# Kernel optimization log

Hardware: AMD Instinct MI355X
Metric: run time of the kernel (lower is better)

## Reference

```python
import jax, jax.numpy as jnp
import numpy as np

N, H, W = 4096, 96, 96
C0 = 0.28209479177387814
C1 = 0.4886025119029199
C2 = [1.0925484305920792, -1.0925484305920792, 0.31539156525252005, -1.0925484305920792, 0.5462742152960396]
C3 = [-0.5900435899266435, 2.890611442640554, -0.4570457994644658, 0.3731763325901154, -0.4570457994644658, 1.445305721320277, -0.5900435899266435]


def setup_inputs() -> dict:
    key = jax.random.key(0)
    ks = jax.random.split(key, 6)
    return {
        'pws': jax.random.normal(ks[0], (N, 3), jnp.float32),
        'low_shs': 0.5 * jax.random.normal(ks[1], (N, 3), jnp.float32),
        'high_shs': 0.1 * jax.random.normal(ks[2], (N, 45), jnp.float32),
        'alphas_raw': jax.random.normal(ks[3], (N, 1), jnp.float32),
        'scales_raw': 0.5 * jax.random.normal(ks[4], (N, 3), jnp.float32) - 3.0,
        'rots_raw': jax.random.normal(ks[5], (N, 4), jnp.float32),
        'us': jnp.zeros((N, 2), jnp.float32),
        'Rcw': jnp.eye(3, dtype=jnp.float32),
        'tcw': jnp.array([0.0, 0.0, 4.0], jnp.float32),
        'cam_intr': jnp.array([120.0, 120.0, 48.0, 48.0], jnp.float32),  # fx fy cx cy
    }


def quat_to_rot(q):
    w, x, y, z = q[:, 0], q[:, 1], q[:, 2], q[:, 3]
    return jnp.stack([
        jnp.stack([1 - 2 * (y * y + z * z), 2 * (x * y - w * z), 2 * (x * z + w * y)], -1),
        jnp.stack([2 * (x * y + w * z), 1 - 2 * (x * x + z * z), 2 * (y * z - w * x)], -1),
        jnp.stack([2 * (x * z - w * y), 2 * (y * z + w * x), 1 - 2 * (x * x + y * y)], -1),
    ], -2)  # [N,3,3]


def sh2color(shs, dirs):
    # shs [N,16,3], dirs [N,3] normalized view directions
    x, y, z = dirs[:, 0:1], dirs[:, 1:2], dirs[:, 2:3]
    xx, yy, zz = x * x, y * y, z * z
    xy, yz, xz = x * y, y * z, x * z
    c = C0 * shs[:, 0]
    c = c - C1 * y * shs[:, 1] + C1 * z * shs[:, 2] - C1 * x * shs[:, 3]
    c = (c + C2[0] * xy * shs[:, 4] + C2[1] * yz * shs[:, 5]
         + C2[2] * (2 * zz - xx - yy) * shs[:, 6]
         + C2[3] * xz * shs[:, 7] + C2[4] * (xx - yy) * shs[:, 8])
    c = (c + C3[0] * y * (3 * xx - yy) * shs[:, 9] + C3[1] * xy * z * shs[:, 10]
         + C3[2] * y * (4 * zz - xx - yy) * shs[:, 11]
         + C3[3] * z * (2 * zz - 3 * xx - 3 * yy) * shs[:, 12]
         + C3[4] * x * (4 * zz - xx - yy) * shs[:, 13]
         + C3[5] * z * (xx - yy) * shs[:, 14]
         + C3[6] * x * (xx - 3 * yy) * shs[:, 15])
    return jnp.maximum(c + 0.5, 0.0)  # [N,3]


def _forward(pws, low_shs, high_shs, alphas_raw, scales_raw, rots_raw, Rcw, tcw, cam_intr):
    fx, fy, cx, cy = cam_intr[0], cam_intr[1], cam_intr[2], cam_intr[3]
    alphas = jax.nn.sigmoid(alphas_raw)[:, 0]                 # get_alphas
    scales = jnp.exp(scales_raw)                              # get_scales
    rots = rots_raw / jnp.linalg.norm(rots_raw, axis=1, keepdims=True)  # get_rots
    shs = jnp.concatenate([low_shs, high_shs], axis=1).reshape(-1, 16, 3)

    # --- project ---
    pcs = pws @ Rcw.T + tcw                                   # [N,3] camera coords
    depths = pcs[:, 2]
    zs = jnp.where(depths > 1e-6, depths, 1e-6)
    u = jnp.stack([fx * pcs[:, 0] / zs + cx, fy * pcs[:, 1] / zs + cy], axis=1)

    # --- cov3d = (R S)(R S)^T ---
    M = quat_to_rot(rots) * scales[:, None, :]
    cov3d = M @ jnp.swapaxes(M, 1, 2)                          # [N,3,3]

    # --- cov2d = J W cov3d W^T J^T + 0.3 I ---
    limx, limy = 1.3 * (W / (2.0 * fx)), 1.3 * (H / (2.0 * fy))
    tx = jnp.clip(pcs[:, 0] / zs, -limx, limx) * zs
    ty = jnp.clip(pcs[:, 1] / zs, -limy, limy) * zs
    zero = jnp.zeros_like(zs)
    J = jnp.stack([
        jnp.stack([fx / zs, zero, -fx * tx / (zs * zs)], -1),
        jnp.stack([zero, fy / zs, -fy * ty / (zs * zs)], -1),
    ], -2)                                                     # [N,2,3]
    T = J @ Rcw
    cov2d = T @ cov3d @ jnp.swapaxes(T, 1, 2)
    a = cov2d[:, 0, 0] + 0.3
    b = cov2d[:, 0, 1]
    c2 = cov2d[:, 1, 1] + 0.3

    # --- inverseCov2D + areas (radius of 3-sigma ellipse) ---
    det = a * c2 - b * b
    cinv = jnp.stack([c2, -b, a], axis=1) / det[:, None]       # [N,3]
    mid = 0.5 * (a + c2)
    lam = mid + jnp.sqrt(jnp.maximum(mid * mid - det, 0.1))
    radius = jnp.ceil(3.0 * jnp.sqrt(lam))
    areas = jnp.stack([radius, radius], axis=1)                # [N,2]

    # --- sh2Color ---
    twc = -(Rcw.T @ tcw)
    dirs = pws - twc
    dirs = dirs / jnp.linalg.norm(dirs, axis=1, keepdims=True)
    colors = sh2color(shs, dirs)                               # [N,3]

    # --- splat: depth-sorted alpha compositing ---
    valid = depths > 0.2
    order = jnp.argsort(depths)
    u_s, cinv_s = u[order], cinv[order]
    alpha_s, color_s, valid_s = alphas[order], colors[order], valid[order]

    px = (jnp.arange(W, dtype=jnp.float32))[None, :].repeat(H, 0).reshape(-1)
    py = (jnp.arange(H, dtype=jnp.float32))[:, None].repeat(W, 1).reshape(-1)
    dx = u_s[:, 0:1] - px[None, :]                             # [N,P]
    dy = u_s[:, 1:2] - py[None, :]
    power = -0.5 * (cinv_s[:, 0:1] * dx * dx + cinv_s[:, 2:3] * dy * dy) - cinv_s[:, 1:2] * dx * dy
    ap = jnp.minimum(alpha_s[:, None] * jnp.exp(jnp.minimum(power, 0.0)), 0.99)
    ap = jnp.where((ap >= 1.0 / 255.0) & valid_s[:, None], ap, 0.0)
    logt = jnp.cumsum(jnp.log1p(-ap), axis=0)
    tau = jnp.exp(jnp.concatenate([jnp.zeros((1, ap.shape[1])), logt[:-1]], axis=0))
    wgt = jnp.where(tau > 1e-4, ap * tau, 0.0)                 # [N,P]
    image = jnp.einsum('nc,np->cp', color_s, wgt).reshape(3, H, W)
    return image, areas


def reference(pws, low_shs, high_shs, alphas_raw, scales_raw, rots_raw, us, Rcw, tcw, cam_intr):
    return _forward(pws, low_shs, high_shs, alphas_raw, scales_raw, rots_raw, Rcw, tcw, cam_intr)
```

## Files before the change

### kernel.cpp

```cpp
#include <hip/hip_runtime.h>
#include <hip/hip_bf16.h>
#include <math.h>

#define GS_N 4096
#define IMG_H 96
#define IMG_W 96
#define NPIX (IMG_H * IMG_W)
#define TILE_PX 12
#define TILES_X 8
#define NTILES (TILES_X * TILES_X)
#define WAVES_PER_TILE 36

#define SH_C0 0.28209479177387814f
#define SH_C1 0.4886025119029199f
__device__ __constant__ float kC2[5] = {1.0925484305920792f, -1.0925484305920792f, 0.31539156525252005f, -1.0925484305920792f, 0.5462742152960396f};
__device__ __constant__ float kC3[7] = {-0.5900435899266435f, 2.890611442640554f, -0.4570457994644658f, 0.3731763325901154f, -0.4570457994644658f, 1.445305721320277f, -0.5900435899266435f};

__device__ __forceinline__ float wave_incl_prod(float x) {
#if __has_builtin(__builtin_amdgcn_update_dpp)
    const int ONE = __float_as_int(1.0f);
    int t;
    t = __builtin_amdgcn_update_dpp(ONE, __float_as_int(x), 0x111, 0xf, 0xf, false);
    x *= __int_as_float(t);
    t = __builtin_amdgcn_update_dpp(ONE, __float_as_int(x), 0x112, 0xf, 0xf, false);
    x *= __int_as_float(t);
    t = __builtin_amdgcn_update_dpp(ONE, __float_as_int(x), 0x114, 0xf, 0xf, false);
    x *= __int_as_float(t);
    t = __builtin_amdgcn_update_dpp(ONE, __float_as_int(x), 0x118, 0xf, 0xf, false);
    x *= __int_as_float(t);
    t = __builtin_amdgcn_update_dpp(ONE, __float_as_int(x), 0x142, 0xa, 0xf, false);
    x *= __int_as_float(t);
    t = __builtin_amdgcn_update_dpp(ONE, __float_as_int(x), 0x143, 0xc, 0xf, false);
    x *= __int_as_float(t);
    return x;
#else
    int lane = threadIdx.x & 63;
    #pragma unroll
    for (int d = 1; d < 64; d <<= 1) {
        float v = __shfl_up(x, d, 64);
        if (lane >= d) x *= v;
    }
    return x;
#endif
}

__global__ __launch_bounds__(256) void gs_prep(
    const float* __restrict__ pws, const float* __restrict__ low_shs,
    const float* __restrict__ high_shs, const float* __restrict__ alphas_raw,
    const float* __restrict__ scales_raw, const float* __restrict__ rots_raw,
    const float* __restrict__ Rcw, const float* __restrict__ tcw,
    const float* __restrict__ cam,
    float* __restrict__ areas_out,
    float* __restrict__ depth_ws,
    int*   __restrict__ rank_ws,
    float4* __restrict__ A_uns,
    float4* __restrict__ B_uns,
    float* __restrict__ C_uns,
    float4* __restrict__ D_uns,
    unsigned long long* __restrict__ mask_ws)
{
    int i = blockIdx.x * 256 + threadIdx.x;
    if (i >= GS_N) return;

    rank_ws[i] = 0;
    mask_ws[i] = 0ull;

    float fx = cam[0], fy = cam[1], cxi = cam[2], cyi = cam[3];
    float R0 = Rcw[0], R1 = Rcw[1], R2 = Rcw[2];
    float R3 = Rcw[3], R4 = Rcw[4], R5 = Rcw[5];
    float R6 = Rcw[6], R7 = Rcw[7], R8 = Rcw[8];
    float t0 = tcw[0], t1 = tcw[1], t2 = tcw[2];

    float pwx = pws[3*i+0], pwy = pws[3*i+1], pwz = pws[3*i+2];

    float pcx = R0*pwx + R1*pwy + R2*pwz + t0;
    float pcy = R3*pwx + R4*pwy + R5*pwz + t1;
    float pcz = R6*pwx + R7*pwy + R8*pwz + t2;

    float depth = pcz;
    float zs = (depth > 1e-6f) ? depth : 1e-6f;

    float ux = fx * pcx / zs + cxi;
    float uy = fy * pcy / zs + cyi;

    float alpha = 1.0f / (1.0f + expf(-alphas_raw[i]));

    float s0 = expf(scales_raw[3*i+0]);
    float s1 = expf(scales_raw[3*i+1]);
    float s2 = expf(scales_raw[3*i+2]);

    float qw = rots_raw[4*i+0], qx = rots_raw[4*i+1], qy = rots_raw[4*i+2], qz = rots_raw[4*i+3];
    float qn = sqrtf(qw*qw + qx*qx + qy*qy + qz*qz);
    qw /= qn; qx /= qn; qy /= qn; qz /= qn;

    float r00 = 1.0f - 2.0f*(qy*qy + qz*qz);
    float r01 = 2.0f*(qx*qy - qw*qz);
    float r02 = 2.0f*(qx*qz + qw*qy);
    float r10 = 2.0f*(qx*qy + qw*qz);
    float r11 = 1.0f - 2.0f*(qx*qx + qz*qz);
    float r12 = 2.0f*(qy*qz - qw*qx);
    float r20 = 2.0f*(qx*qz - qw*qy);
    float r21 = 2.0f*(qy*qz + qw*qx);
    float r22 = 1.0f - 2.0f*(qx*qx + qy*qy);

    float m00 = r00*s0, m01 = r01*s1, m02 = r02*s2;
    float m10 = r10*s0, m11 = r11*s1, m12 = r12*s2;
    float m20 = r20*s0, m21 = r21*s1, m22 = r22*s2;

    float V00 = m00*m00 + m01*m01 + m02*m02;
    float V01 = m00*m10 + m01*m11 + m02*m12;
    float V02 = m00*m20 + m01*m21 + m02*m22;
    float V11 = m10*m10 + m11*m11 + m12*m12;
    float V12 = m10*m20 + m11*m21 + m12*m22;
    float V22 = m20*m20 + m21*m21 + m22*m22;

    float limx = 1.3f * ((float)IMG_W / (2.0f * fx));
    float limy = 1.3f * ((float)IMG_H / (2.0f * fy));
    float xzr = pcx / zs, yzr = pcy / zs;
    float txv = fminf(fmaxf(xzr, -limx), limx) * zs;
    float tyv = fminf(fmaxf(yzr, -limy), limy) * zs;

    float J00 = fx / zs, J02 = -fx * txv / (zs * zs);
    float J11 = fy / zs, J12 = -fy * tyv / (zs * zs);

    float T00 = J00*R0 + J02*R6, T01 = J00*R1 + J02*R7, T02 = J00*R2 + J02*R8;
    float T10 = J11*R3 + J12*R6, T11 = J11*R4 + J12*R7, T12 = J11*R5 + J12*R8;

    float TW00 = T00*V00 + T01*V01 + T02*V02;
    float TW01 = T00*V01 + T01*V11 + T02*V12;
    float TW02 = T00*V02 + T01*V12 + T02*V22;
    float TW10 = T10*V00 + T11*V01 + T12*V02;
    float TW11 = T10*V01 + T11*V11 + T12*V12;
    float TW12 = T10*V02 + T11*V12 + T12*V22;

    float c00 = TW00*T00 + TW01*T01 + TW02*T02;
    float c01 = TW00*T10 + TW01*T11 + TW02*T12;
    float c11 = TW10*T10 + TW11*T11 + TW12*T12;

    float a  = c00 + 0.3f;
    float b  = c01;
    float cc = c11 + 0.3f;
    float det = a * cc - b * b;
    float ci0 = cc / det;
    float ci1 = -b / det;
    float ci2 = a / det;

    float mid = 0.5f * (a + cc);
    float lam = mid + sqrtf(fmaxf(mid * mid - det, 0.1f));
    float radius = ceilf(3.0f * sqrtf(lam));
    areas_out[2*i + 0] = radius;
    areas_out[2*i + 1] = radius;

    float twcx = -(R0*t0 + R3*t1 + R6*t2);
    float twcy = -(R1*t0 + R4*t1 + R7*t2);
    float twcz = -(R2*t0 + R5*t1 + R8*t2);
    float dx = pwx - twcx, dy = pwy - twcy, dz = pwz - twcz;
    float dn = sqrtf(dx*dx + dy*dy + dz*dz);
    dx /= dn; dy /= dn; dz /= dn;

    float xx = dx*dx, yy = dy*dy, zz = dz*dz;
    float xy = dx*dy, yz = dy*dz, xz = dx*dz;

    float bas0  = SH_C0;
    float bas1  = -SH_C1 * dy;
    float bas2  =  SH_C1 * dz;
    float bas3  = -SH_C1 * dx;
    float bas4  = kC2[0] * xy;
    float bas5  = kC2[1] * yz;
    float bas6  = kC2[2] * (2.0f*zz - xx - yy);
    float bas7  = kC2[3] * xz;
    float bas8  = kC2[4] * (xx - yy);
    float bas9  = kC3[0] * dy * (3.0f*xx - yy);
    float bas10 = kC3[1] * xy * dz;
    float bas11 = kC3[2] * dy * (4.0f*zz - xx - yy);
    float bas12 = kC3[3] * dz * (2.0f*zz - 3.0f*xx - 3.0f*yy);
    float bas13 = kC3[4] * dx * (4.0f*zz - xx - yy);
    float bas14 = kC3[5] * dz * (xx - yy);
    float bas15 = kC3[6] * dx * (xx - 3.0f*yy);

    float col[3];
    #pragma unroll
    for (int c = 0; c < 3; ++c) {
        const float* hs = high_shs + 45*i + c;
        float acc = bas0 * low_shs[3*i + c];
        acc += bas1  * hs[0*3];
        acc += bas2  * hs[1*3];
        acc += bas3  * hs[2*3];
        acc += bas4  * hs[3*3];
        acc += bas5  * hs[4*3];
        acc += bas6  * hs[5*3];
        acc += bas7  * hs[6*3];
        acc += bas8  * hs[7*3];
        acc += bas9  * hs[8*3];
        acc += bas10 * hs[9*3];
        acc += bas11 * hs[10*3];
        acc += bas12 * hs[11*3];
        acc += bas13 * hs[12*3];
        acc += bas14 * hs[13*3];
        acc += bas15 * hs[14*3];
        col[c] = fmaxf(acc + 0.5f, 0.0f);
    }

    bool valid = depth > 0.2f;
    float al_eff = valid ? alpha : 0.0f;

    float Tthr = __logf(255.0f * al_eff) + 1e-4f;
    float rx = (Tthr > 0.0f) ? sqrtf(2.0f * Tthr * a)  : -1.0f;
    float ry = (Tthr > 0.0f) ? sqrtf(2.0f * Tthr * cc) : -1.0f;

    depth_ws[i] = depth;
    A_uns[i] = make_float4(ux, uy, ci0, ci1);
    B_uns[i] = make_float4(ci2, al_eff, col[0], col[1]);
    C_uns[i] = col[2];
    D_uns[i] = make_float4(ux, uy, rx, ry);
}

__global__ __launch_bounds__(256) void gs_rank_partial(
    const float* __restrict__ depth, int* __restrict__ rank_ws)
{
    __shared__ float sd[256];
    int itile = blockIdx.x >> 4;
    int jtile = blockIdx.x & 15;
    int tid = threadIdx.x;
    int i = itile * 256 + tid;

    sd[tid] = depth[jtile * 256 + tid];
    __syncthreads();

    float mg = depth[i];
    int jbase = jtile * 256;
    int rank = 0;
    const float4* s4 = (const float4*)sd;
    #pragma unroll 16
    for (int jj = 0; jj < 64; ++jj) {
        float4 v = s4[jj];
        int j0 = jbase + jj * 4;
        rank += (v.x < mg || (v.x == mg && (j0+0) < i)) ? 1 : 0;
        rank += (v.y < mg || (v.y == mg && (j0+1) < i)) ? 1 : 0;
        rank += (v.z < mg || (v.z == mg && (j0+2) < i)) ? 1 : 0;
        rank += (v.w < mg || (v.w == mg && (j0+3) < i)) ? 1 : 0;
    }
    atomicAdd(&rank_ws[i], rank);
}

__global__ __launch_bounds__(256) void gs_gather_mask(
    const int* __restrict__ rank_ws,
    const float4* __restrict__ D_uns,
    int* __restrict__ inv_ws,
    unsigned long long* __restrict__ mask_ws)
{
    int i = blockIdx.x * 256 + threadIdx.x;
    int r = rank_ws[i];
    inv_ws[r] = i;

    float4 d = D_uns[i];
    if (d.z >= 0.0f) {
        const float inv = 1.0f / (float)TILE_PX;
        int tx0 = max(0, (int)ceilf((d.x - d.z - (float)(TILE_PX - 1)) * inv - 1e-4f));
        int tx1 = min(TILES_X - 1, (int)floorf((d.x + d.z) * inv + 1e-4f));
        int ty0 = max(0, (int)ceilf((d.y - d.w - (float)(TILE_PX - 1)) * inv - 1e-4f));
        int ty1 = min(TILES_X - 1, (int)floorf((d.y + d.w) * inv + 1e-4f));
        unsigned long long bit = 1ull << (r & 63);
        int w = r >> 6;
        for (int ty = ty0; ty <= ty1; ++ty)
            for (int tx = tx0; tx <= tx1; ++tx)
                atomicOr(&mask_ws[(ty * TILES_X + tx) * 64 + w], bit);
    }
}

__global__ __launch_bounds__(256) void gs_expand(
    const unsigned long long* __restrict__ mask_ws,
    const int* __restrict__ inv_ws,
    const float4* __restrict__ A_uns, const float4* __restrict__ B_uns,
    const float* __restrict__ C_uns,
    float4* __restrict__ E_A, float4* __restrict__ E_B, float* __restrict__ E_C,
    int* __restrict__ tile_cnt)
{
    __shared__ unsigned short slist[GS_N];
    __shared__ int scnt;

    int tile = blockIdx.x;
    int tid = threadIdx.x;
    int lane = tid & 63, wv = tid >> 6;

    if (wv == 0) {
        unsigned long long m = mask_ws[tile * 64 + lane];
        int c = __popcll(m);
        int incl = c;
        #pragma unroll
        for (int d = 1; d < 64; d <<= 1) {
            int v = __shfl_up(incl, d, 64);
            if (lane >= d) incl += v;
        }
        int off = incl - c;
        int base = lane << 6;
        while (m) {
            int bpos = __builtin_ctzll(m);
            m &= m - 1;
            slist[off++] = (unsigned short)(base + bpos);
        }
        if (lane == 63) { scnt = incl; tile_cnt[tile] = incl; }
    }
    __syncthreads();
    int cnt = scnt;

    float4* tA = E_A + tile * GS_N;
    float4* tB = E_B + tile * GS_N;
    float*  tC = E_C + tile * GS_N;
    for (int k = tid; k < cnt; k += 256) {
        int n = inv_ws[slist[k]];
        tA[k] = A_uns[n];
        tB[k] = B_uns[n];
        tC[k] = C_uns[n];
    }
}

__global__ __launch_bounds__(256) void gs_raster(
    const float4* __restrict__ E_A, const float4* __restrict__ E_B,
    const float* __restrict__ E_C,
    const int* __restrict__ tile_cnt,
    float* __restrict__ img)
{
    int b = blockIdx.x;
    int tile = b / WAVES_PER_TILE;
    int sub  = b - tile * WAVES_PER_TILE;
    int lane = threadIdx.x & 63;
    int wv   = threadIdx.x >> 6;

    int idxp = sub * 4 + wv;
    int lx = idxp % TILE_PX, ly = idxp / TILE_PX;
    int tx = tile & (TILES_X - 1), ty = tile >> 3;
    int pxi = tx * TILE_PX + lx, pyi = ty * TILE_PX + ly;
    float px = (float)pxi, py = (float)pyi;
    int p = pyi * IMG_W + pxi;

    int cnt = tile_cnt[tile];
    const float4* tA = E_A + tile * GS_N;
    const float4* tB = E_B + tile * GS_N;
    const float*  tC = E_C + tile * GS_N;

    float carry = 1.0f;
    float accr = 0.0f, accg = 0.0f, accb = 0.0f;

    for (int c0 = 0; c0 < cnt; c0 += 128) {
        int k0 = c0 + (lane << 1);
        float ap0 = 0.0f, r0 = 0.0f, g0 = 0.0f, b0 = 0.0f;
        float ap1 = 0.0f, r1 = 0.0f, g1 = 0.0f, b1 = 0.0f;
        if (k0 < cnt) {
            float4 a4 = tA[k0];
            float4 b4 = tB[k0];
            b0 = tC[k0]; r0 = b4.z; g0 = b4.w;
            float ddx = a4.x - px, ddy = a4.y - py;
            float pw = -0.5f * (a4.z * ddx * ddx + b4.x * ddy * ddy) - a4.w * ddx * ddy;
            pw = fminf(pw, 0.0f);
            ap0 = b4.y * __expf(pw);
            ap0 = fminf(ap0, 0.99f);
            ap0 = (ap0 >= (1.0f / 255.0f)) ? ap0 : 0.0f;
        }
        if (k0 + 1 < cnt) {
            float4 a4 = tA[k0 + 1];
            float4 b4 = tB[k0 + 1];
            b1 = tC[k0 + 1]; r1 = b4.z; g1 = b4.w;
            float ddx = a4.x - px, ddy = a4.y - py;
            float pw = -0.5f * (a4.z * ddx * ddx + b4.x * ddy * ddy) - a4.w * ddx * ddy;
            pw = fminf(pw, 0.0f);
            ap1 = b4.y * __expf(pw);
            ap1 = fminf(ap1, 0.99f);
            ap1 = (ap1 >= (1.0f / 255.0f)) ? ap1 : 0.0f;
        }

        if (__ballot(ap0 > 0.0f || ap1 > 0.0f) == 0ull) continue;

        float f0 = 1.0f - ap0;
        float f1 = 1.0f - ap1;
        float incl = wave_incl_prod(f0 * f1);
        float excl = __shfl_up(incl, 1, 64);
        excl = (lane == 0) ? 1.0f : excl;

        float tau0 = carry * excl;
        float tau1 = tau0 * f0;
        float w0 = (tau0 > 1e-4f) ? ap0 * tau0 : 0.0f;
        float w1 = (tau1 > 1e-4f) ? ap1 * tau1 : 0.0f;
        accr += r0 * w0 + r1 * w1;
        accg += g0 * w0 + g1 * w1;
        accb += b0 * w0 + b1 * w1;

        carry *= __shfl(incl, 63, 64);
        if (carry <= 1e-4f) break;
    }

    #pragma unroll
    for (int d = 32; d >= 1; d >>= 1) {
        accr += __shfl_xor(accr, d, 64);
        accg += __shfl_xor(accg, d, 64);
        accb += __shfl_xor(accb, d, 64);
    }
    if (lane == 0) {
        img[0 * NPIX + p] = accr;
        img[1 * NPIX + p] = accg;
        img[2 * NPIX + p] = accb;
    }
}

extern "C" void kernel_launch(void* const* d_in, const int* in_sizes, int n_in,
                              void* d_out, int out_size, void* d_ws, size_t ws_size,
                              hipStream_t stream) {
    const float* pws        = (const float*)d_in[0];
    const float* low_shs    = (const float*)d_in[1];
    const float* high_shs   = (const float*)d_in[2];
    const float* alphas_raw = (const float*)d_in[3];
    const float* scales_raw = (const float*)d_in[4];
    const float* rots_raw   = (const float*)d_in[5];
    const float* Rcw        = (const float*)d_in[7];
    const float* tcw        = (const float*)d_in[8];
    const float* cam        = (const float*)d_in[9];

    float* out_img   = (float*)d_out;
    float* out_areas = (float*)d_out + 3 * NPIX;

    char* ws = (char*)d_ws;
    float*  depth_ws = (float*) (ws + 0);
    int*    rank_ws  = (int*)   (ws + 16384);
    int*    inv_ws   = (int*)   (ws + 32768);
    float4* A_uns    = (float4*)(ws + 49152);
    float4* B_uns    = (float4*)(ws + 114688);
    float*  C_uns    = (float*) (ws + 180224);
    float4* D_uns    = (float4*)(ws + 196608);
    unsigned long long* mask_ws = (unsigned long long*)(ws + 262144);
    float4* E_A      = (float4*)(ws + 294912);
    float4* E_B      = (float4*)(ws + 4489216);
    float*  E_C      = (float*) (ws + 8683520);
    int*    tile_cnt = (int*)   (ws + 9732096);

    gs_prep<<<GS_N / 256, 256, 0, stream>>>(
        pws, low_shs, high_shs, alphas_raw, scales_raw, rots_raw, Rcw, tcw, cam,
        out_areas, depth_ws, rank_ws, A_uns, B_uns, C_uns, D_uns, mask_ws);

    gs_rank_partial<<<256, 256, 0, stream>>>(depth_ws, rank_ws);

    gs_gather_mask<<<GS_N / 256, 256, 0, stream>>>(
        rank_ws, D_uns, inv_ws, mask_ws);

    gs_expand<<<NTILES, 256, 0, stream>>>(
        mask_ws, inv_ws, A_uns, B_uns, C_uns, E_A, E_B, E_C, tile_cnt);

    gs_raster<<<NTILES * WAVES_PER_TILE, 256, 0, stream>>>(
        E_A, E_B, E_C, tile_cnt, out_img);
}
```

Before: 94.76 us.

## Fuse rank/mask via last-block counter and gather per-tile lists inside raster

Merges the rank and mask kernels into one, using a per-row done counter so the last block of each row scatters the inverse permutation and sets the tile bitmasks. Drops the expand kernel and its sorted per-tile copies. Each raster block now rebuilds its tile's index list from the bitmask in shared memory and reads gaussian data indirectly through inv_ws. This removes two launches and the large expanded buffers, at the cost of rebuilding the list 36 times per tile and doing dependent indirect loads in the raster loop.

```diff
diff --git a/kernel.cpp b/kernel.cpp
--- a/kernel.cpp
+++ b/kernel.cpp
@@ -53,6 +53,7 @@
     float* __restrict__ areas_out,
     float* __restrict__ depth_ws,
     int*   __restrict__ rank_ws,
+    int*   __restrict__ done_ws,
     float4* __restrict__ A_uns,
     float4* __restrict__ B_uns,
     float* __restrict__ C_uns,
@@ -64,6 +65,7 @@
 
     rank_ws[i] = 0;
     mask_ws[i] = 0ull;
+    if (i < 16) done_ws[i] = 0;
 
     float fx = cam[0], fy = cam[1], cxi = cam[2], cyi = cam[3];
     float R0 = Rcw[0], R1 = Rcw[1], R2 = Rcw[2];
@@ -215,10 +217,13 @@
     D_uns[i] = make_float4(ux, uy, rx, ry);
 }
 
-__global__ __launch_bounds__(256) void gs_rank_partial(
-    const float* __restrict__ depth, int* __restrict__ rank_ws)
+__global__ __launch_bounds__(256) void gs_rank_mask(
+    const float* __restrict__ depth, const float4* __restrict__ D_uns,
+    int* __restrict__ rank_ws, int* __restrict__ done_ws,
+    int* __restrict__ inv_ws, unsigned long long* __restrict__ mask_ws)
 {
     __shared__ float sd[256];
+    __shared__ int is_last;
     int itile = blockIdx.x >> 4;
     int jtile = blockIdx.x & 15;
     int tid = threadIdx.x;
@@ -241,16 +246,17 @@
         rank += (v.w < mg || (v.w == mg && (j0+3) < i)) ? 1 : 0;
     }
     atomicAdd(&rank_ws[i], rank);
-}
-
-__global__ __launch_bounds__(256) void gs_gather_mask(
-    const int* __restrict__ rank_ws,
-    const float4* __restrict__ D_uns,
-    int* __restrict__ inv_ws,
-    unsigned long long* __restrict__ mask_ws)
-{
-    int i = blockIdx.x * 256 + threadIdx.x;
-    int r = rank_ws[i];
+    __threadfence();
+    __syncthreads();
+    if (tid == 0) {
+        int old = atomicAdd(&done_ws[itile], 1);
+        is_last = (old == 15);
+    }
+    __syncthreads();
+    if (!is_last) return;
+
+    __threadfence();
+    int r = __hip_atomic_load(&rank_ws[i], __ATOMIC_RELAXED, __HIP_MEMORY_SCOPE_AGENT);
     inv_ws[r] = i;
 
     float4 d = D_uns[i];
@@ -268,20 +274,21 @@
     }
 }
 
-__global__ __launch_bounds__(256) void gs_expand(
-    const unsigned long long* __restrict__ mask_ws,
-    const int* __restrict__ inv_ws,
+__global__ __launch_bounds__(256) void gs_raster(
     const float4* __restrict__ A_uns, const float4* __restrict__ B_uns,
     const float* __restrict__ C_uns,
-    float4* __restrict__ E_A, float4* __restrict__ E_B, float* __restrict__ E_C,
-    int* __restrict__ tile_cnt)
+    const int* __restrict__ inv_ws,
+    const unsigned long long* __restrict__ mask_ws,
+    float* __restrict__ img)
 {
     __shared__ unsigned short slist[GS_N];
     __shared__ int scnt;
 
-    int tile = blockIdx.x;
-    int tid = threadIdx.x;
-    int lane = tid & 63, wv = tid >> 6;
+    int b = blockIdx.x;
+    int tile = b / WAVES_PER_TILE;
+    int sub  = b - tile * WAVES_PER_TILE;
+    int lane = threadIdx.x & 63;
+    int wv   = threadIdx.x >> 6;
 
     if (wv == 0) {
         unsigned long long m = mask_ws[tile * 64 + lane];
@@ -299,33 +306,10 @@
             m &= m - 1;
             slist[off++] = (unsigned short)(base + bpos);
         }
-        if (lane == 63) { scnt = incl; tile_cnt[tile] = incl; }
+        if (lane == 63) scnt = incl;
     }
     __syncthreads();
     int cnt = scnt;
-
-    float4* tA = E_A + tile * GS_N;
-    float4* tB = E_B + tile * GS_N;
-    float*  tC = E_C + tile * GS_N;
-    for (int k = tid; k < cnt; k += 256) {
-        int n = inv_ws[slist[k]];
-        tA[k] = A_uns[n];
-        tB[k] = B_uns[n];
-        tC[k] = C_uns[n];
-    }
-}
-
-__global__ __launch_bounds__(256) void gs_raster(
-    const float4* __restrict__ E_A, const float4* __restrict__ E_B,
-    const float* __restrict__ E_C,
-    const int* __restrict__ tile_cnt,
-    float* __restrict__ img)
-{
-    int b = blockIdx.x;
-    int tile = b / WAVES_PER_TILE;
-    int sub  = b - tile * WAVES_PER_TILE;
-    int lane = threadIdx.x & 63;
-    int wv   = threadIdx.x >> 6;
 
     int idxp = sub * 4 + wv;
     int lx = idxp % TILE_PX, ly = idxp / TILE_PX;
@@ -334,11 +318,6 @@
     float px = (float)pxi, py = (float)pyi;
     int p = pyi * IMG_W + pxi;
 
-    int cnt = tile_cnt[tile];
-    const float4* tA = E_A + tile * GS_N;
-    const float4* tB = E_B + tile * GS_N;
-    const float*  tC = E_C + tile * GS_N;
-
     float carry = 1.0f;
     float accr = 0.0f, accg = 0.0f, accb = 0.0f;
 
@@ -347,9 +326,10 @@
         float ap0 = 0.0f, r0 = 0.0f, g0 = 0.0f, b0 = 0.0f;
         float ap1 = 0.0f, r1 = 0.0f, g1 = 0.0f, b1 = 0.0f;
         if (k0 < cnt) {
-            float4 a4 = tA[k0];
-            float4 b4 = tB[k0];
-            b0 = tC[k0]; r0 = b4.z; g0 = b4.w;
+            int n = inv_ws[slist[k0]];
+            float4 a4 = A_uns[n];
+            float4 b4 = B_uns[n];
+            b0 = C_uns[n]; r0 = b4.z; g0 = b4.w;
             float ddx = a4.x - px, ddy = a4.y - py;
             float pw = -0.5f * (a4.z * ddx * ddx + b4.x * ddy * ddy) - a4.w * ddx * ddy;
             pw = fminf(pw, 0.0f);
@@ -358,9 +338,10 @@
             ap0 = (ap0 >= (1.0f / 255.0f)) ? ap0 : 0.0f;
         }
         if (k0 + 1 < cnt) {
-            float4 a4 = tA[k0 + 1];
-            float4 b4 = tB[k0 + 1];
-            b1 = tC[k0 + 1]; r1 = b4.z; g1 = b4.w;
+            int n = inv_ws[slist[k0 + 1]];
+            float4 a4 = A_uns[n];
+            float4 b4 = B_uns[n];
+            b1 = C_uns[n]; r1 = b4.z; g1 = b4.w;
             float ddx = a4.x - px, ddy = a4.y - py;
             float pw = -0.5f * (a4.z * ddx * ddx + b4.x * ddy * ddy) - a4.w * ddx * ddy;
             pw = fminf(pw, 0.0f);
@@ -427,23 +408,15 @@
     float*  C_uns    = (float*) (ws + 180224);
     float4* D_uns    = (float4*)(ws + 196608);
     unsigned long long* mask_ws = (unsigned long long*)(ws + 262144);
-    float4* E_A      = (float4*)(ws + 294912);
-    float4* E_B      = (float4*)(ws + 4489216);
-    float*  E_C      = (float*) (ws + 8683520);
-    int*    tile_cnt = (int*)   (ws + 9732096);
+    int*    done_ws  = (int*)   (ws + 294912);
 
     gs_prep<<<GS_N / 256, 256, 0, stream>>>(
         pws, low_shs, high_shs, alphas_raw, scales_raw, rots_raw, Rcw, tcw, cam,
-        out_areas, depth_ws, rank_ws, A_uns, B_uns, C_uns, D_uns, mask_ws);
-
-    gs_rank_partial<<<256, 256, 0, stream>>>(depth_ws, rank_ws);
-
-    gs_gather_mask<<<GS_N / 256, 256, 0, stream>>>(
-        rank_ws, D_uns, inv_ws, mask_ws);
-
-    gs_expand<<<NTILES, 256, 0, stream>>>(
-        mask_ws, inv_ws, A_uns, B_uns, C_uns, E_A, E_B, E_C, tile_cnt);
+        out_areas, depth_ws, rank_ws, done_ws, A_uns, B_uns, C_uns, D_uns, mask_ws);
+
+    gs_rank_mask<<<256, 256, 0, stream>>>(
+        depth_ws, D_uns, rank_ws, done_ws, inv_ws, mask_ws);
 
     gs_raster<<<NTILES * WAVES_PER_TILE, 256, 0, stream>>>(
-        E_A, E_B, E_C, tile_cnt, out_img);
+        A_uns, B_uns, C_uns, inv_ws, mask_ws, out_img);
 }
```

After: 115.8 us. 1.22x slower.

## Fuse rank and mask kernels; stage high SH coefficients through shared memory

Applied to the files above, without the earlier changes.

Merges the depth-rank counting and the gather/tile-mask kernels into one kernel. Each block loads all depths into shared memory, 16 lanes split one Gaussian's comparisons, and the partial counts are reduced with wave shuffles. This removes the rank atomics, the rank workspace and one kernel launch. The prep kernel also copies each block's 45-float SH rows into shared memory with coalesced loads instead of strided per-thread global reads. The cost is a 45 KB shared-memory footprint per prep block and redundant full-depth loads in each of the 256 rank blocks.

```diff
diff --git a/kernel.cpp b/kernel.cpp
--- a/kernel.cpp
+++ b/kernel.cpp
@@ -52,17 +52,22 @@
     const float* __restrict__ cam,
     float* __restrict__ areas_out,
     float* __restrict__ depth_ws,
-    int*   __restrict__ rank_ws,
     float4* __restrict__ A_uns,
     float4* __restrict__ B_uns,
     float* __restrict__ C_uns,
     float4* __restrict__ D_uns,
     unsigned long long* __restrict__ mask_ws)
 {
-    int i = blockIdx.x * 256 + threadIdx.x;
+    __shared__ float shlds[256 * 45];
+    int tid = threadIdx.x;
+    int gbase = blockIdx.x * 256 * 45;
+    #pragma unroll
+    for (int k = tid; k < 256 * 45; k += 256) shlds[k] = high_shs[gbase + k];
+    __syncthreads();
+
+    int i = blockIdx.x * 256 + tid;
     if (i >= GS_N) return;
 
-    rank_ws[i] = 0;
     mask_ws[i] = 0ull;
 
     float fx = cam[0], fy = cam[1], cxi = cam[2], cyi = cam[3];
@@ -178,10 +183,11 @@
     float bas14 = kC3[5] * dz * (xx - yy);
     float bas15 = kC3[6] * dx * (xx - 3.0f*yy);
 
+    const float* hs0 = shlds + 45 * tid;
     float col[3];
     #pragma unroll
     for (int c = 0; c < 3; ++c) {
-        const float* hs = high_shs + 45*i + c;
+        const float* hs = hs0 + c;
         float acc = bas0 * low_shs[3*i + c];
         acc += bas1  * hs[0*3];
         acc += bas2  * hs[1*3];
@@ -215,56 +221,52 @@
     D_uns[i] = make_float4(ux, uy, rx, ry);
 }
 
-__global__ __launch_bounds__(256) void gs_rank_partial(
-    const float* __restrict__ depth, int* __restrict__ rank_ws)
+__global__ __launch_bounds__(256) void gs_rankmask(
+    const float* __restrict__ depth, const float4* __restrict__ D_uns,
+    int* __restrict__ inv_ws, unsigned long long* __restrict__ mask_ws)
 {
-    __shared__ float sd[256];
-    int itile = blockIdx.x >> 4;
-    int jtile = blockIdx.x & 15;
+    __shared__ float sd[GS_N];
     int tid = threadIdx.x;
-    int i = itile * 256 + tid;
-
-    sd[tid] = depth[jtile * 256 + tid];
+    #pragma unroll
+    for (int k = tid; k < GS_N; k += 256) sd[k] = depth[k];
     __syncthreads();
 
-    float mg = depth[i];
-    int jbase = jtile * 256;
+    int g    = blockIdx.x * 16 + (tid >> 4);
+    int part = tid & 15;
+    float mg = sd[g];
+
+    int jbase = part * 256;
+    const float4* s4 = (const float4*)(sd + jbase);
     int rank = 0;
-    const float4* s4 = (const float4*)sd;
-    #pragma unroll 16
+    #pragma unroll 8
     for (int jj = 0; jj < 64; ++jj) {
         float4 v = s4[jj];
         int j0 = jbase + jj * 4;
-        rank += (v.x < mg || (v.x == mg && (j0+0) < i)) ? 1 : 0;
-        rank += (v.y < mg || (v.y == mg && (j0+1) < i)) ? 1 : 0;
-        rank += (v.z < mg || (v.z == mg && (j0+2) < i)) ? 1 : 0;
-        rank += (v.w < mg || (v.w == mg && (j0+3) < i)) ? 1 : 0;
-    }
-    atomicAdd(&rank_ws[i], rank);
-}
-
-__global__ __launch_bounds__(256) void gs_gather_mask(
-    const int* __restrict__ rank_ws,
-    const float4* __restrict__ D_uns,
-    int* __restrict__ inv_ws,
-    unsigned long long* __restrict__ mask_ws)
-{
-    int i = blockIdx.x * 256 + threadIdx.x;
-    int r = rank_ws[i];
-    inv_ws[r] = i;
-
-    float4 d = D_uns[i];
-    if (d.z >= 0.0f) {
-        const float inv = 1.0f / (float)TILE_PX;
-        int tx0 = max(0, (int)ceilf((d.x - d.z - (float)(TILE_PX - 1)) * inv - 1e-4f));
-        int tx1 = min(TILES_X - 1, (int)floorf((d.x + d.z) * inv + 1e-4f));
-        int ty0 = max(0, (int)ceilf((d.y - d.w - (float)(TILE_PX - 1)) * inv - 1e-4f));
-        int ty1 = min(TILES_X - 1, (int)floorf((d.y + d.w) * inv + 1e-4f));
-        unsigned long long bit = 1ull << (r & 63);
-        int w = r >> 6;
-        for (int ty = ty0; ty <= ty1; ++ty)
-            for (int tx = tx0; tx <= tx1; ++tx)
-                atomicOr(&mask_ws[(ty * TILES_X + tx) * 64 + w], bit);
+        rank += (v.x < mg || (v.x == mg && (j0+0) < g)) ? 1 : 0;
+        rank += (v.y < mg || (v.y == mg && (j0+1) < g)) ? 1 : 0;
+        rank += (v.z < mg || (v.z == mg && (j0+2) < g)) ? 1 : 0;
+        rank += (v.w < mg || (v.w == mg && (j0+3) < g)) ? 1 : 0;
+    }
+    rank += __shfl_xor(rank, 1, 64);
+    rank += __shfl_xor(rank, 2, 64);
+    rank += __shfl_xor(rank, 4, 64);
+    rank += __shfl_xor(rank, 8, 64);
+
+    if (part == 0) {
+        inv_ws[rank] = g;
+        float4 d = D_uns[g];
+        if (d.z >= 0.0f) {
+            const float inv = 1.0f / (float)TILE_PX;
+            int tx0 = max(0, (int)ceilf((d.x - d.z - (float)(TILE_PX - 1)) * inv - 1e-4f));
+            int tx1 = min(TILES_X - 1, (int)floorf((d.x + d.z) * inv + 1e-4f));
+            int ty0 = max(0, (int)ceilf((d.y - d.w - (float)(TILE_PX - 1)) * inv - 1e-4f));
+            int ty1 = min(TILES_X - 1, (int)floorf((d.y + d.w) * inv + 1e-4f));
+            unsigned long long bit = 1ull << (rank & 63);
+            int w = rank >> 6;
+            for (int ty = ty0; ty <= ty1; ++ty)
+                for (int tx = tx0; tx <= tx1; ++tx)
+                    atomicOr(&mask_ws[(ty * TILES_X + tx) * 64 + w], bit);
+        }
     }
 }
 
@@ -420,26 +422,23 @@
 
     char* ws = (char*)d_ws;
     float*  depth_ws = (float*) (ws + 0);
-    int*    rank_ws  = (int*)   (ws + 16384);
-    int*    inv_ws   = (int*)   (ws + 32768);
-    float4* A_uns    = (float4*)(ws + 49152);
-    float4* B_uns    = (float4*)(ws + 114688);
-    float*  C_uns    = (float*) (ws + 180224);
-    float4* D_uns    = (float4*)(ws + 196608);
-    unsigned long long* mask_ws = (unsigned long long*)(ws + 262144);
-    float4* E_A      = (float4*)(ws + 294912);
-    float4* E_B      = (float4*)(ws + 4489216);
-    float*  E_C      = (float*) (ws + 8683520);
-    int*    tile_cnt = (int*)   (ws + 9732096);
+    int*    inv_ws   = (int*)   (ws + 16384);
+    float4* A_uns    = (float4*)(ws + 32768);
+    float4* B_uns    = (float4*)(ws + 98304);
+    float*  C_uns    = (float*) (ws + 163840);
+    float4* D_uns    = (float4*)(ws + 180224);
+    unsigned long long* mask_ws = (unsigned long long*)(ws + 245760);
+    float4* E_A      = (float4*)(ws + 278528);
+    float4* E_B      = (float4*)(ws + 4472832);
+    float*  E_C      = (float*) (ws + 8667136);
+    int*    tile_cnt = (int*)   (ws + 9715712);
 
     gs_prep<<<GS_N / 256, 256, 0, stream>>>(
         pws, low_shs, high_shs, alphas_raw, scales_raw, rots_raw, Rcw, tcw, cam,
-        out_areas, depth_ws, rank_ws, A_uns, B_uns, C_uns, D_uns, mask_ws);
-
-    gs_rank_partial<<<256, 256, 0, stream>>>(depth_ws, rank_ws);
-
-    gs_gather_mask<<<GS_N / 256, 256, 0, stream>>>(
-        rank_ws, D_uns, inv_ws, mask_ws);
+        out_areas, depth_ws, A_uns, B_uns, C_uns, D_uns, mask_ws);
+
+    gs_rankmask<<<GS_N / 16, 256, 0, stream>>>(
+        depth_ws, D_uns, inv_ws, mask_ws);
 
     gs_expand<<<NTILES, 256, 0, stream>>>(
         mask_ws, inv_ws, A_uns, B_uns, C_uns, E_A, E_B, E_C, tile_cnt);
```

Result: slower. 102.4 us (+8.1%).
